# Kernel tuning notes

Measured on AMD Instinct MI355X. Metric: run time of the kernel, lower is better.

Reference implementation:

```python
import jax, jax.numpy as jnp
import numpy as np

B, N, FIN, FOUT, K = 8, 1024, 32, 4, 2
FREQS = [2.0, 3.0, 4.0, 5.0]  # q_idx = 1/FREQS[idx]


def setup_inputs() -> dict:
    key = jax.random.key(0)
    k1, k2, k3, k4, k5 = jax.random.split(key, 5)
    X_real = jax.random.normal(k1, (B, N, FIN), jnp.float32)
    X_imag = jax.random.normal(k2, (B, N, FIN), jnp.float32)
    adj = jax.random.uniform(k3, (B, N, N), jnp.float32)  # weighted directed adjacency
    stdv = 1.0 / np.sqrt(FIN)
    weight = jax.random.uniform(k4, (FOUT, K + 1, FIN), jnp.float32, -stdv, stdv)
    bias = jax.random.uniform(k5, (FOUT,), jnp.float32, -stdv, stdv)
    return {"X_real": X_real, "X_imag": X_imag, "adj": adj, "weight": weight, "bias": bias}


def _mag_laplacian(adj, q):
    """Normalized magnetic Laplacian, real/imag parts. adj: [B,N,N]."""
    adj_t = jnp.swapaxes(adj, -1, -2)
    As = 0.5 * (adj + adj_t)                    # symmetrized adjacency
    D = As.sum(-1)                              # degrees [B,N]
    dinv = jnp.where(D > 0, 1.0 / jnp.sqrt(jnp.where(D > 0, D, 1.0)), 0.0)
    theta = (2.0 * np.pi * q) * (adj - adj_t)   # phase matrix
    S = dinv[:, :, None] * As * dinv[:, None, :]  # D^-1/2 As D^-1/2
    I = jnp.eye(N, dtype=adj.dtype)
    L_real = I - S * jnp.cos(theta)
    L_imag = -S * jnp.sin(theta)
    return L_real, L_imag


def _cmatvec(Lr, Li, zr, zi):
    """Complex batched matmul (Lr+iLi) @ (zr+izi); L:[B,N,N], z:[B,N,F]."""
    return Lr @ zr - Li @ zi, Li @ zr + Lr @ zi


def reference(X_real, X_imag, adj, weight, bias):
    outs_r, outs_i = [], []
    for idx in range(FOUT):  # small fixed loop over output channels / frequencies
        q = 1.0 / FREQS[idx]
        Lr, Li = _mag_laplacian(adj, q)
        # Chebyshev polynomials applied directly to the signal:
        # T0 = I -> z0 = X ; T1 = I - L -> z1 = X - L X ; T_k = 2 L T_{k-1} + T_{k-2}
        z = [(X_real, X_imag)]
        hr, hi = _cmatvec(Lr, Li, X_real, X_imag)
        z.append((X_real - hr, X_imag - hi))
        for i in range(2, K + 1):
            mr, mi = _cmatvec(Lr, Li, z[i - 1][0], z[i - 1][1])
            z.append((2.0 * mr + z[i - 2][0], 2.0 * mi + z[i - 2][1]))
        Zr = jnp.stack([t[0] for t in z], 0)  # [K+1, B, N, FIN]
        Zi = jnp.stack([t[1] for t in z], 0)
        or_ = jnp.einsum('kbnf,kf->bn', Zr, weight[idx]) + bias[idx]
        oi_ = jnp.einsum('kbnf,kf->bn', Zi, weight[idx])
        outs_r.append(or_)
        outs_i.append(oi_)
    return jnp.stack(outs_r, -1), jnp.stack(outs_i, -1)  # each [B, N, FOUT]
```

## Files before the change

kernel.cpp:

```cpp
#include <hip/hip_runtime.h>
#include <cstddef>

#define NB 8
#define NN 1024
#define NF 32
#define NIDX 4

#define OFF_ROW   0u
#define OFF_COLP  8192u
#define OFF_S     8192u
#define OFF_P     (8192u + 65536u)
#define OFF_R     (8192u + 131072u)
#define OFF_DINV  532480u
#define OFF_WT    540672u
#define OFF_WP    606208u

#if __has_builtin(__builtin_amdgcn_sinf)
#define FSIN(x) __builtin_amdgcn_sinf(x)
#define FCOS(x) __builtin_amdgcn_cosf(x)
#else
#define FSIN(x) __sinf((x) * 6.283185307179586f)
#define FCOS(x) __cosf((x) * 6.283185307179586f)
#endif

__global__ __launch_bounds__(512) void k_sums(const float* __restrict__ adj,
                                              float* __restrict__ rowsum,
                                              float* __restrict__ colpart) {
  int b = blockIdx.x, strip = blockIdx.y;
  int t = threadIdx.x, lane = t & 63, w = t >> 6;
  float colreg[16];
  #pragma unroll
  for (int i = 0; i < 16; ++i) colreg[i] = 0.f;
  int r0 = strip*16 + w*2;
  #pragma unroll
  for (int rr = 0; rr < 2; ++rr) {
    const float4* row4 = reinterpret_cast<const float4*>(adj + ((size_t)b*NN + r0 + rr)*NN);
    float rs = 0.f;
    #pragma unroll
    for (int cq = 0; cq < 4; ++cq) {
      float4 v = row4[cq*64 + lane];
      colreg[cq*4+0] += v.x; colreg[cq*4+1] += v.y;
      colreg[cq*4+2] += v.z; colreg[cq*4+3] += v.w;
      rs += (v.x + v.y) + (v.z + v.w);
    }
    #pragma unroll
    for (int o = 32; o > 0; o >>= 1) rs += __shfl_xor(rs, o);
    if (lane == 0) rowsum[b*NN + r0 + rr] = rs;
  }
  __shared__ float cacc[8][NN];
  #pragma unroll
  for (int cq = 0; cq < 4; ++cq)
    #pragma unroll
    for (int x = 0; x < 4; ++x) cacc[w][cq*256 + lane*4 + x] = colreg[cq*4+x];
  __syncthreads();
  for (int c = t; c < NN; c += 512) {
    float s = 0.f;
    #pragma unroll
    for (int ww = 0; ww < 8; ++ww) s += cacc[ww][c];
    colpart[(size_t)strip*(NB*NN) + b*NN + c] = s;
  }
}

__global__ void k_dinv(const float* __restrict__ rowsum, const float* __restrict__ colpart,
                       float* __restrict__ dinv) {
  int g = blockIdx.x*256 + threadIdx.x;
  float cs = 0.f;
  for (int k = 0; k < 64; ++k) cs += colpart[(size_t)k*(NB*NN) + g];
  float D = 0.5f*(rowsum[g] + cs);
  dinv[g] = (D > 0.f) ? (1.0f / sqrtf(D)) : 0.f;
}

__global__ __launch_bounds__(256) void k_prep(const float* __restrict__ Xr, const float* __restrict__ Xi,
                       const float* __restrict__ weight, const float* __restrict__ dinv,
                       float* __restrict__ svec, float* __restrict__ pvec, float* __restrict__ rvec) {
  __shared__ float wsm[NIDX*3*NF];
  int t = threadIdx.x;
  for (int e = t; e < NIDX*3*NF; e += 256) wsm[e] = weight[e];
  __syncthreads();
  int gid = blockIdx.x*256 + t;
  const float* xr = Xr + (size_t)gid*NF;
  const float* xi = Xi + (size_t)gid*NF;
  float acc[NIDX][3][2];
  #pragma unroll
  for (int x = 0; x < NIDX; ++x)
    #pragma unroll
    for (int v = 0; v < 3; ++v) { acc[x][v][0] = 0.f; acc[x][v][1] = 0.f; }
  for (int f = 0; f < NF; ++f) {
    float xrf = xr[f], xif = xi[f];
    #pragma unroll
    for (int x = 0; x < NIDX; ++x) {
      float w0 = wsm[x*96 + f], w1 = wsm[x*96 + 32 + f], w2 = wsm[x*96 + 64 + f];
      float av = w0 + w2, bv = w1 + 2.f*w2, cv = -2.f*w2;
      acc[x][0][0] += av*xrf; acc[x][0][1] += av*xif;
      acc[x][1][0] += bv*xrf; acc[x][1][1] += bv*xif;
      acc[x][2][0] += cv*xrf; acc[x][2][1] += cv*xif;
    }
  }
  float dj = dinv[gid];
  #pragma unroll
  for (int x = 0; x < NIDX; ++x) {
    size_t o = (size_t)gid*8 + x*2;
    svec[o] = acc[x][0][0];      svec[o+1] = acc[x][0][1];
    pvec[o] = acc[x][1][0];      pvec[o+1] = acc[x][1][1];
    rvec[o] = dj*acc[x][2][0];   rvec[o+1] = dj*acc[x][2][1];
  }
}

__global__ __launch_bounds__(256, 4) void k_pass(const float* __restrict__ adj,
                                                 const float* __restrict__ dinv,
                                                 const float* __restrict__ vin,
                                                 float* __restrict__ outp,
                                                 int jchunk) {
  __shared__ float Arow[64*65];
  __shared__ float red[4][64][9];
  int b = blockIdx.y, i0 = blockIdx.x*64;
  int t = threadIdx.x, lane = t & 63;
  int wu = __builtin_amdgcn_readfirstlane(t >> 6);
  int j0base = blockIdx.z * jchunk;
  const float QV[NIDX] = {0.5f, 1.f/3.f, 0.25f, 0.2f};
  float accr[NIDX], acci[NIDX];
  #pragma unroll
  for (int x = 0; x < NIDX; ++x) { accr[x] = 0.f; acci[x] = 0.f; }

  int njt = jchunk >> 6;
  for (int jt = 0; jt < njt; ++jt) {
    int j0 = j0base + jt*64;
    __syncthreads();
    #pragma unroll
    for (int m = 0; m < 4; ++m) {
      int e4 = t + 256*m;
      int si = e4 >> 4, sj = (e4 & 15) << 2;
      float4 v = *reinterpret_cast<const float4*>(adj + ((size_t)b*NN + i0 + si)*NN + j0 + sj);
      float* dst = &Arow[si*65 + sj];
      dst[0] = v.x; dst[1] = v.y; dst[2] = v.z; dst[3] = v.w;
    }
    __syncthreads();
    const float* acbase = adj + ((size_t)b*NN + j0 + wu*16)*NN + i0 + lane;
    const float* vbase  = vin + ((size_t)(b*NN) + j0 + wu*16)*8;
    const float* abase  = &Arow[lane*65 + wu*16];
    #pragma unroll 4
    for (int k = 0; k < 16; ++k) {
      float ac = acbase[(size_t)k*NN];
      float ar = abase[k];
      float dd = ar - ac;
      float sm = ar + ac;
      float4 v01 = *reinterpret_cast<const float4*>(vbase + k*8);
      float4 v23 = *reinterpret_cast<const float4*>(vbase + k*8 + 4);
      float vr[NIDX] = {v01.x, v01.z, v23.x, v23.z};
      float vi[NIDX] = {v01.y, v01.w, v23.y, v23.w};
      #pragma unroll
      for (int x = 0; x < NIDX; ++x) {
        float u = QV[x]*dd;
        float sn = FSIN(u), cs = FCOS(u);
        float Mr = sm*cs, Mi = sm*sn;
        accr[x] += Mr*vr[x] - Mi*vi[x];
        acci[x] += Mr*vi[x] + Mi*vr[x];
      }
    }
  }
  #pragma unroll
  for (int x = 0; x < NIDX; ++x) {
    red[wu][lane][x*2]   = accr[x];
    red[wu][lane][x*2+1] = acci[x];
  }
  __syncthreads();
  for (int e = t; e < 64*8; e += 256) {
    int ii = e >> 3, s = e & 7;
    float sum = red[0][ii][s] + red[1][ii][s] + red[2][ii][s] + red[3][ii][s];
    sum *= 0.5f * dinv[b*NN + i0 + ii];
    outp[(size_t)blockIdx.z*(NB*NN*8) + ((size_t)(b*NN) + i0 + ii)*8 + s] = sum;
  }
}

__global__ void k_comb(const float* __restrict__ dinv, const float* __restrict__ p,
                       const float* __restrict__ wp, float* __restrict__ wt, int JC) {
  int o4 = blockIdx.x*256 + threadIdx.x;
  float4 a = reinterpret_cast<const float4*>(p)[o4];
  for (int c = 0; c < JC; ++c) {
    float4 v = reinterpret_cast<const float4*>(wp)[(size_t)c*16384 + o4];
    a.x += v.x; a.y += v.y; a.z += v.z; a.w += v.w;
  }
  float dj = dinv[o4 >> 1];
  a.x *= dj; a.y *= dj; a.z *= dj; a.w *= dj;
  reinterpret_cast<float4*>(wt)[o4] = a;
}

__global__ void k_finish(const float* __restrict__ svec, const float* __restrict__ yp,
                         const float* __restrict__ bias, float* __restrict__ out, int JC) {
  int wI = blockIdx.x*256 + threadIdx.x;
  int idx = wI & 3, gid = wI >> 2;
  size_t o = (size_t)gid*8 + idx*2;
  float re = svec[o], im = svec[o+1];
  for (int c = 0; c < JC; ++c) {
    re += yp[(size_t)c*65536 + o];
    im += yp[(size_t)c*65536 + o + 1];
  }
  out[wI] = re + bias[idx];
  out[32768 + wI] = im;
}

extern "C" void kernel_launch(void* const* d_in, const int* in_sizes, int n_in,
                              void* d_out, int out_size, void* d_ws, size_t ws_size,
                              hipStream_t stream) {
  (void)in_sizes; (void)n_in; (void)out_size;
  const float* Xr     = (const float*)d_in[0];
  const float* Xi     = (const float*)d_in[1];
  const float* adj    = (const float*)d_in[2];
  const float* weight = (const float*)d_in[3];
  const float* bias   = (const float*)d_in[4];
  float* ws = (float*)d_ws;
  float* rowsum  = ws + OFF_ROW;
  float* colpart = ws + OFF_COLP;
  float* svec    = ws + OFF_S;
  float* pvec    = ws + OFF_P;
  float* rvec    = ws + OFF_R;
  float* dinv    = ws + OFF_DINV;
  float* wtot    = ws + OFF_WT;
  float* wpart   = ws + OFF_WP;
  float* out = (float*)d_out;

  int JC = 2;
  if (ws_size >= (size_t)(OFF_WP + 8u*65536u)*4u)      JC = 8;
  else if (ws_size >= (size_t)(OFF_WP + 4u*65536u)*4u) JC = 4;

  k_sums<<<dim3(NB, 64), 512, 0, stream>>>(adj, rowsum, colpart);
  k_dinv<<<dim3(NB*NN/256), 256, 0, stream>>>(rowsum, colpart, dinv);
  k_prep<<<dim3(NB*NN/256), 256, 0, stream>>>(Xr, Xi, weight, dinv, svec, pvec, rvec);
  k_pass<<<dim3(NN/64, NB, JC), 256, 0, stream>>>(adj, dinv, rvec, wpart, NN/JC);
  k_comb<<<dim3(64), 256, 0, stream>>>(dinv, pvec, wpart, wtot, JC);
  k_pass<<<dim3(NN/64, NB, JC), 256, 0, stream>>>(adj, dinv, wtot, wpart, NN/JC);
  k_finish<<<dim3(NB*NN*NIDX/256), 256, 0, stream>>>(svec, wpart, bias, out, JC);
}
```

Before: 65.55 us.

## Fuse dinv, combine and finish stages into neighbouring kernels and retile the pass

Folds the degree/dinv kernel into k_prep and the partial-sum combine and finish kernels into the two Laplacian pass kernels. The second pass reduces its j-chunks by atomicAdd into an output that k_sums zeroes. The pass kernel is restructured to 512 threads, with each thread accumulating 8 rows and a shuffle-based transpose reduction. The adj row is read from global memory and the transpose tile is staged in LDS. Fewer launches and less partial-buffer traffic come at the cost of higher register pressure, float atomics and a fixed JC of 4.

```diff
diff --git a/kernel.cpp b/kernel.cpp
--- a/kernel.cpp
+++ b/kernel.cpp
@@ -5,15 +5,17 @@
 #define NN 1024
 #define NF 32
 #define NIDX 4
+#define JC 4
+#define JCH 256
+#define NJT 4
 
 #define OFF_ROW   0u
 #define OFF_COLP  8192u
-#define OFF_S     8192u
-#define OFF_P     (8192u + 65536u)
-#define OFF_R     (8192u + 131072u)
 #define OFF_DINV  532480u
-#define OFF_WT    540672u
-#define OFF_WP    606208u
+#define OFF_S     540672u
+#define OFF_P     606208u
+#define OFF_R     671744u
+#define OFF_WP    737280u
 
 #if __has_builtin(__builtin_amdgcn_sinf)
 #define FSIN(x) __builtin_amdgcn_sinf(x)
@@ -25,9 +27,12 @@
 
 __global__ __launch_bounds__(512) void k_sums(const float* __restrict__ adj,
                                               float* __restrict__ rowsum,
-                                              float* __restrict__ colpart) {
+                                              float* __restrict__ colpart,
+                                              float* __restrict__ out) {
   int b = blockIdx.x, strip = blockIdx.y;
   int t = threadIdx.x, lane = t & 63, w = t >> 6;
+  { int zid = blockIdx.x*64 + blockIdx.y;
+    if (t < 128) out[zid*128 + t] = 0.f; }
   float colreg[16];
   #pragma unroll
   for (int i = 0; i < 16; ++i) colreg[i] = 0.f;
@@ -61,23 +66,21 @@
   }
 }
 
-__global__ void k_dinv(const float* __restrict__ rowsum, const float* __restrict__ colpart,
-                       float* __restrict__ dinv) {
-  int g = blockIdx.x*256 + threadIdx.x;
-  float cs = 0.f;
-  for (int k = 0; k < 64; ++k) cs += colpart[(size_t)k*(NB*NN) + g];
-  float D = 0.5f*(rowsum[g] + cs);
-  dinv[g] = (D > 0.f) ? (1.0f / sqrtf(D)) : 0.f;
-}
-
 __global__ __launch_bounds__(256) void k_prep(const float* __restrict__ Xr, const float* __restrict__ Xi,
-                       const float* __restrict__ weight, const float* __restrict__ dinv,
+                       const float* __restrict__ weight,
+                       const float* __restrict__ rowsum, const float* __restrict__ colpart,
+                       float* __restrict__ dinv,
                        float* __restrict__ svec, float* __restrict__ pvec, float* __restrict__ rvec) {
   __shared__ float wsm[NIDX*3*NF];
   int t = threadIdx.x;
   for (int e = t; e < NIDX*3*NF; e += 256) wsm[e] = weight[e];
   __syncthreads();
   int gid = blockIdx.x*256 + t;
+  float cs = 0.f;
+  for (int k = 0; k < 64; ++k) cs += colpart[(size_t)k*(NB*NN) + gid];
+  float D = 0.5f*(rowsum[gid] + cs);
+  float di = (D > 0.f) ? (1.0f / sqrtf(D)) : 0.f;
+  dinv[gid] = di;
   const float* xr = Xr + (size_t)gid*NF;
   const float* xi = Xi + (size_t)gid*NF;
   float acc[NIDX][3][2];
@@ -96,113 +99,137 @@
       acc[x][2][0] += cv*xrf; acc[x][2][1] += cv*xif;
     }
   }
-  float dj = dinv[gid];
   #pragma unroll
   for (int x = 0; x < NIDX; ++x) {
     size_t o = (size_t)gid*8 + x*2;
     svec[o] = acc[x][0][0];      svec[o+1] = acc[x][0][1];
     pvec[o] = acc[x][1][0];      pvec[o+1] = acc[x][1][1];
-    rvec[o] = dj*acc[x][2][0];   rvec[o+1] = dj*acc[x][2][1];
-  }
-}
-
-__global__ __launch_bounds__(256, 4) void k_pass(const float* __restrict__ adj,
+    rvec[o] = di*acc[x][2][0];   rvec[o+1] = di*acc[x][2][1];
+  }
+}
+
+template<int MODE>
+__global__ __launch_bounds__(512, 4) void k_pass(const float* __restrict__ adj,
                                                  const float* __restrict__ dinv,
                                                  const float* __restrict__ vin,
-                                                 float* __restrict__ outp,
-                                                 int jchunk) {
-  __shared__ float Arow[64*65];
-  __shared__ float red[4][64][9];
-  int b = blockIdx.y, i0 = blockIdx.x*64;
+                                                 float* __restrict__ wpart,
+                                                 const float* __restrict__ svec,
+                                                 const float* __restrict__ bias,
+                                                 float* __restrict__ out) {
+  __shared__ float Tjs[64][65];
+  __shared__ float vlds[JCH][8];
+  __shared__ float red[8][8*72];
+  int b = blockIdx.y, i0 = blockIdx.x*64, zc = blockIdx.z;
+  int j0base = zc*JCH;
   int t = threadIdx.x, lane = t & 63;
-  int wu = __builtin_amdgcn_readfirstlane(t >> 6);
-  int j0base = blockIdx.z * jchunk;
+  int w = t >> 6;
+  int wu = __builtin_amdgcn_readfirstlane(w);
   const float QV[NIDX] = {0.5f, 1.f/3.f, 0.25f, 0.2f};
-  float accr[NIDX], acci[NIDX];
-  #pragma unroll
-  for (int x = 0; x < NIDX; ++x) { accr[x] = 0.f; acci[x] = 0.f; }
-
-  int njt = jchunk >> 6;
-  for (int jt = 0; jt < njt; ++jt) {
+
+  if constexpr (MODE == 1) {
+    for (int e = t; e < JCH*8; e += 512) {
+      int jj = e >> 3, s = e & 7;
+      size_t o = ((size_t)b*NN + j0base + jj)*8 + s;
+      float v = vin[o];
+      #pragma unroll
+      for (int c = 0; c < JC; ++c) v += wpart[(size_t)c*65536 + o];
+      vlds[jj][s] = v * dinv[b*NN + j0base + jj];
+    }
+  }
+
+  float accr[8][NIDX], acci[8][NIDX];
+  #pragma unroll
+  for (int s = 0; s < 8; ++s)
+    #pragma unroll
+    for (int x = 0; x < NIDX; ++x) { accr[s][x] = 0.f; acci[s][x] = 0.f; }
+
+  for (int jt = 0; jt < NJT; ++jt) {
     int j0 = j0base + jt*64;
     __syncthreads();
     #pragma unroll
-    for (int m = 0; m < 4; ++m) {
-      int e4 = t + 256*m;
-      int si = e4 >> 4, sj = (e4 & 15) << 2;
-      float4 v = *reinterpret_cast<const float4*>(adj + ((size_t)b*NN + i0 + si)*NN + j0 + sj);
-      float* dst = &Arow[si*65 + sj];
-      dst[0] = v.x; dst[1] = v.y; dst[2] = v.z; dst[3] = v.w;
+    for (int m = 0; m < 2; ++m) {
+      int e4 = t + 512*m;
+      int jj = e4 >> 4, i4 = (e4 & 15) << 2;
+      float4 vv = *reinterpret_cast<const float4*>(adj + ((size_t)b*NN + j0 + jj)*NN + i0 + i4);
+      float* dst = &Tjs[jj][i4];
+      dst[0] = vv.x; dst[1] = vv.y; dst[2] = vv.z; dst[3] = vv.w;
+    }
+    float vr[NIDX], vi[NIDX];
+    if constexpr (MODE == 0) {
+      const float4* vb = reinterpret_cast<const float4*>(vin + ((size_t)b*NN + j0 + lane)*8);
+      float4 a = vb[0], c = vb[1];
+      vr[0]=a.x; vi[0]=a.y; vr[1]=a.z; vi[1]=a.w;
+      vr[2]=c.x; vi[2]=c.y; vr[3]=c.z; vi[3]=c.w;
+    } else {
+      const float4* vb = reinterpret_cast<const float4*>(&vlds[jt*64 + lane][0]);
+      float4 a = vb[0], c = vb[1];
+      vr[0]=a.x; vi[0]=a.y; vr[1]=a.z; vi[1]=a.w;
+      vr[2]=c.x; vi[2]=c.y; vr[3]=c.z; vi[3]=c.w;
     }
     __syncthreads();
-    const float* acbase = adj + ((size_t)b*NN + j0 + wu*16)*NN + i0 + lane;
-    const float* vbase  = vin + ((size_t)(b*NN) + j0 + wu*16)*8;
-    const float* abase  = &Arow[lane*65 + wu*16];
-    #pragma unroll 4
-    for (int k = 0; k < 16; ++k) {
-      float ac = acbase[(size_t)k*NN];
-      float ar = abase[k];
-      float dd = ar - ac;
-      float sm = ar + ac;
-      float4 v01 = *reinterpret_cast<const float4*>(vbase + k*8);
-      float4 v23 = *reinterpret_cast<const float4*>(vbase + k*8 + 4);
-      float vr[NIDX] = {v01.x, v01.z, v23.x, v23.z};
-      float vi[NIDX] = {v01.y, v01.w, v23.y, v23.w};
+    const float* arbase = adj + ((size_t)b*NN + i0 + wu*8)*NN + j0 + lane;
+    #pragma unroll
+    for (int s = 0; s < 8; ++s) {
+      float ar = arbase[(size_t)s*NN];
+      float ac = Tjs[lane][wu*8 + s];
+      float dd = ar - ac, sm = ar + ac;
       #pragma unroll
       for (int x = 0; x < NIDX; ++x) {
         float u = QV[x]*dd;
-        float sn = FSIN(u), cs = FCOS(u);
-        float Mr = sm*cs, Mi = sm*sn;
-        accr[x] += Mr*vr[x] - Mi*vi[x];
-        acci[x] += Mr*vi[x] + Mi*vr[x];
+        float sn = FSIN(u), cw = FCOS(u);
+        float tr = cw*vr[x] - sn*vi[x];
+        float ti = cw*vi[x] + sn*vr[x];
+        accr[s][x] += sm*tr;
+        acci[s][x] += sm*ti;
       }
     }
   }
-  #pragma unroll
-  for (int x = 0; x < NIDX; ++x) {
-    red[wu][lane][x*2]   = accr[x];
-    red[wu][lane][x*2+1] = acci[x];
+
+  bool b1 = (lane & 1), b2 = (lane & 2), b4 = (lane & 4);
+  #pragma unroll
+  for (int s = 0; s < 8; ++s) {
+    float v0 = accr[s][0], v1 = acci[s][0], v2 = accr[s][1], v3 = acci[s][1];
+    float v4 = accr[s][2], v5 = acci[s][2], v6 = accr[s][3], v7 = acci[s][3];
+    float k0 = b1 ? v1 : v0, s0 = b1 ? v0 : v1;
+    float k1 = b1 ? v3 : v2, s1 = b1 ? v2 : v3;
+    float k2 = b1 ? v5 : v4, s2 = b1 ? v4 : v5;
+    float k3 = b1 ? v7 : v6, s3 = b1 ? v6 : v7;
+    v0 = k0 + __shfl_xor(s0, 1);
+    v1 = k1 + __shfl_xor(s1, 1);
+    v2 = k2 + __shfl_xor(s2, 1);
+    v3 = k3 + __shfl_xor(s3, 1);
+    k0 = b2 ? v1 : v0; s0 = b2 ? v0 : v1;
+    k1 = b2 ? v3 : v2; s1 = b2 ? v2 : v3;
+    v0 = k0 + __shfl_xor(s0, 2);
+    v1 = k1 + __shfl_xor(s1, 2);
+    k0 = b4 ? v1 : v0; s0 = b4 ? v0 : v1;
+    v0 = k0 + __shfl_xor(s0, 4);
+    red[w][s*72 + (lane & 7)*9 + (lane >> 3)] = v0;
   }
   __syncthreads();
-  for (int e = t; e < 64*8; e += 256) {
-    int ii = e >> 3, s = e & 7;
-    float sum = red[0][ii][s] + red[1][ii][s] + red[2][ii][s] + red[3][ii][s];
-    sum *= 0.5f * dinv[b*NN + i0 + ii];
-    outp[(size_t)blockIdx.z*(NB*NN*8) + ((size_t)(b*NN) + i0 + ii)*8 + s] = sum;
-  }
-}
-
-__global__ void k_comb(const float* __restrict__ dinv, const float* __restrict__ p,
-                       const float* __restrict__ wp, float* __restrict__ wt, int JC) {
-  int o4 = blockIdx.x*256 + threadIdx.x;
-  float4 a = reinterpret_cast<const float4*>(p)[o4];
-  for (int c = 0; c < JC; ++c) {
-    float4 v = reinterpret_cast<const float4*>(wp)[(size_t)c*16384 + o4];
-    a.x += v.x; a.y += v.y; a.z += v.z; a.w += v.w;
-  }
-  float dj = dinv[o4 >> 1];
-  a.x *= dj; a.y *= dj; a.z *= dj; a.w *= dj;
-  reinterpret_cast<float4*>(wt)[o4] = a;
-}
-
-__global__ void k_finish(const float* __restrict__ svec, const float* __restrict__ yp,
-                         const float* __restrict__ bias, float* __restrict__ out, int JC) {
-  int wI = blockIdx.x*256 + threadIdx.x;
-  int idx = wI & 3, gid = wI >> 2;
-  size_t o = (size_t)gid*8 + idx*2;
-  float re = svec[o], im = svec[o+1];
-  for (int c = 0; c < JC; ++c) {
-    re += yp[(size_t)c*65536 + o];
-    im += yp[(size_t)c*65536 + o + 1];
-  }
-  out[wI] = re + bias[idx];
-  out[32768 + wI] = im;
+  {
+    int iloc = w*8 + (lane >> 3), slot = lane & 7;
+    float sum = 0.f;
+    #pragma unroll
+    for (int g = 0; g < 8; ++g) sum += red[w][(lane >> 3)*72 + slot*9 + g];
+    int i = i0 + iloc;
+    float val = sum * 0.5f * dinv[b*NN + i];
+    if constexpr (MODE == 0) {
+      wpart[(size_t)zc*65536 + ((size_t)b*NN + i)*8 + slot] = val;
+    } else {
+      if (zc == 0) {
+        val += svec[((size_t)b*NN + i)*8 + slot];
+        if ((slot & 1) == 0) val += bias[slot >> 1];
+      }
+      atomicAdd(&out[(slot & 1)*32768 + b*4096 + i*4 + (slot >> 1)], val);
+    }
+  }
 }
 
 extern "C" void kernel_launch(void* const* d_in, const int* in_sizes, int n_in,
                               void* d_out, int out_size, void* d_ws, size_t ws_size,
                               hipStream_t stream) {
-  (void)in_sizes; (void)n_in; (void)out_size;
+  (void)in_sizes; (void)n_in; (void)out_size; (void)ws_size;
   const float* Xr     = (const float*)d_in[0];
   const float* Xi     = (const float*)d_in[1];
   const float* adj    = (const float*)d_in[2];
@@ -211,23 +238,15 @@
   float* ws = (float*)d_ws;
   float* rowsum  = ws + OFF_ROW;
   float* colpart = ws + OFF_COLP;
+  float* dinv    = ws + OFF_DINV;
   float* svec    = ws + OFF_S;
   float* pvec    = ws + OFF_P;
   float* rvec    = ws + OFF_R;
-  float* dinv    = ws + OFF_DINV;
-  float* wtot    = ws + OFF_WT;
   float* wpart   = ws + OFF_WP;
   float* out = (float*)d_out;
 
-  int JC = 2;
-  if (ws_size >= (size_t)(OFF_WP + 8u*65536u)*4u)      JC = 8;
-  else if (ws_size >= (size_t)(OFF_WP + 4u*65536u)*4u) JC = 4;
-
-  k_sums<<<dim3(NB, 64), 512, 0, stream>>>(adj, rowsum, colpart);
-  k_dinv<<<dim3(NB*NN/256), 256, 0, stream>>>(rowsum, colpart, dinv);
-  k_prep<<<dim3(NB*NN/256), 256, 0, stream>>>(Xr, Xi, weight, dinv, svec, pvec, rvec);
-  k_pass<<<dim3(NN/64, NB, JC), 256, 0, stream>>>(adj, dinv, rvec, wpart, NN/JC);
-  k_comb<<<dim3(64), 256, 0, stream>>>(dinv, pvec, wpart, wtot, JC);
-  k_pass<<<dim3(NN/64, NB, JC), 256, 0, stream>>>(adj, dinv, wtot, wpart, NN/JC);
-  k_finish<<<dim3(NB*NN*NIDX/256), 256, 0, stream>>>(svec, wpart, bias, out, JC);
-}
+  k_sums<<<dim3(NB, 64), 512, 0, stream>>>(adj, rowsum, colpart, out);
+  k_prep<<<dim3(NB*NN/256), 256, 0, stream>>>(Xr, Xi, weight, rowsum, colpart, dinv, svec, pvec, rvec);
+  k_pass<0><<<dim3(NN/64, NB, JC), 512, 0, stream>>>(adj, dinv, rvec, wpart, svec, bias, out);
+  k_pass<1><<<dim3(NN/64, NB, JC), 512, 0, stream>>>(adj, dinv, pvec, wpart, svec, bias, out);
+}
```

New measurement: 56.18 us. -14.3%, faster.
